# Kernel tuning notes

Measured on AMD Instinct MI355X. Metric: run time of the kernel, lower is better.

The kernel has to match this reference:

```python
import jax, jax.numpy as jnp
import numpy as np

K = 8192      # codebook_dim
D = 256       # embedding_dim
BETA = 0.25
DECAY = 0.99
EPS = 1e-05


def setup_inputs() -> dict:
    key = jax.random.key(0)
    k1, k2, k3, k4 = jax.random.split(key, 4)
    lim = 1.0 / K
    return {
        "z": jax.random.normal(k1, (8, D, 32, 32), dtype=jnp.float32),
        "embedding": jax.random.uniform(k2, (K, D), minval=-lim, maxval=lim, dtype=jnp.float32),
        "cluster_size": jax.random.uniform(k3, (K,), dtype=jnp.float32),
        "ema_w": jax.random.uniform(k4, (K, D), minval=-lim, maxval=lim, dtype=jnp.float32),
    }


def reference(z, embedding, cluster_size, ema_w):
    # z: [B, C, H, W] -> [B, H, W, C]
    zp = jnp.transpose(z, (0, 2, 3, 1))
    zf = zp.reshape(-1, D)                                  # [N, D]
    # squared L2 distance to each code: ||z||^2 + ||e||^2 - 2 z.e
    d = (jnp.sum(zf * zf, axis=1, keepdims=True)
         + jnp.sum(embedding * embedding, axis=1)
         - 2.0 * jnp.einsum("nd,kd->nk", zf, embedding))    # [N, K]
    idx = jnp.argmin(d, axis=1)                             # [N]
    z_q = embedding[idx].reshape(zp.shape)                  # [B, H, W, C]

    # EMA update (training branch), expressed with segment sums instead of
    # materializing the one-hot [N, K] matrix.
    counts = jax.ops.segment_sum(jnp.ones_like(idx, dtype=zf.dtype), idx, num_segments=K)
    new_cs = cluster_size * DECAY + (1.0 - DECAY) * counts
    n = jnp.sum(new_cs)
    new_cs = (new_cs + EPS) / (n + K * EPS) * n
    dw = jax.ops.segment_sum(zf, idx, num_segments=K)       # encodings.T @ zf
    new_ema_w = ema_w * DECAY + (1.0 - DECAY) * dw
    new_embedding = new_ema_w / new_cs[:, None]

    sg = jax.lax.stop_gradient
    loss = jnp.mean((sg(z_q) - zp) ** 2) + BETA * jnp.mean((z_q - sg(zp)) ** 2)
    # straight-through estimator, back to NCHW
    z_q_out = jnp.transpose(zp + sg(z_q - zp), (0, 3, 1, 2))
    return z_q_out, loss, idx, new_cs, new_ema_w, new_embedding
```

## Files before the change

kernel.cpp:

```cpp
#include <hip/hip_runtime.h>

#define CHW 262144
#define HWD 1024

typedef _Float16 v8h __attribute__((ext_vector_type(8)));
typedef _Float16 v4h __attribute__((ext_vector_type(4)));
typedef float    v4f __attribute__((ext_vector_type(4)));

static const unsigned OFF_ASQ  = 0;
static const unsigned OFF_BSQ  = 8192;
static const unsigned OFF_CNT  = 16384;
static const unsigned OFF_HEAD = 24576;
static const unsigned OFF_SCAL = 32768;
static const unsigned OFF_NXT  = 32776;
static const unsigned OFF_ZF   = 40968;
static const unsigned OFF_BH   = 2138120;
static const unsigned OFF_PDK  = 3186696;

#define GLL(g, l) __builtin_amdgcn_global_load_lds( \
    (const __attribute__((address_space(1))) void*)(g), \
    (__attribute__((address_space(3))) void*)(l), 16, 0, 0)

__global__ __launch_bounds__(256) void k_prep(const float* __restrict__ z,
        const float* __restrict__ emb, float* __restrict__ asq, float* __restrict__ bsq,
        _Float16* __restrict__ Bh, _Float16* __restrict__ Bm,
        _Float16* __restrict__ Ah, _Float16* __restrict__ Am,
        float* __restrict__ zf32, float* __restrict__ zerobase) {
    int bx = blockIdx.x;
    int t = threadIdx.x;
    if (bx < 32) {
        int n = bx * 256 + t;
        const float* p = z + (size_t)(n >> 10) * CHW + (n & 1023);
        float s = 0.f;
        #pragma unroll 8
        for (int c = 0; c < 256; ++c) { float v = p[(size_t)c << 10]; s = fmaf(v, v, s); }
        asq[n] = s;
    } else if (bx < 2080) {
        int w = (bx - 32) * 4 + (t >> 6);
        int lane = t & 63;
        float4 v = *(const float4*)(emb + (size_t)w * 256 + lane * 4);
        float s = v.x * v.x;
        s = fmaf(v.y, v.y, s); s = fmaf(v.z, v.z, s); s = fmaf(v.w, v.w, s);
        #pragma unroll
        for (int m = 1; m < 64; m <<= 1) s += __shfl_xor(s, m, 64);
        if (lane == 0) bsq[w] = s;
        float e0 = v.x * 8192.0f, e1 = v.y * 8192.0f, e2 = v.z * 8192.0f, e3 = v.w * 8192.0f;
        _Float16 h0 = (_Float16)e0, h1 = (_Float16)e1, h2 = (_Float16)e2, h3 = (_Float16)e3;
        v4h hv = {h0, h1, h2, h3};
        v4h mv = {(_Float16)((e0 - (float)h0) * 2048.0f),
                  (_Float16)((e1 - (float)h1) * 2048.0f),
                  (_Float16)((e2 - (float)h2) * 2048.0f),
                  (_Float16)((e3 - (float)h3) * 2048.0f)};
        *(v4h*)(Bh + (size_t)w * 256 + lane * 4) = hv;
        *(v4h*)(Bm + (size_t)w * 256 + lane * 4) = mv;
    } else if (bx < 2592) {
        __shared__ float s[64][65];
        int blk = bx - 2080;
        int hw0 = (blk & 15) * 64;
        int c0  = ((blk >> 4) & 3) * 64;
        int b   = blk >> 6;
        #pragma unroll
        for (int ii = 0; ii < 16; ++ii) {
            int e = t + ii * 256;
            int c = e >> 6, x = e & 63;
            s[c][x] = z[(size_t)b * CHW + (size_t)(c0 + c) * HWD + hw0 + x];
        }
        __syncthreads();
        int n = t & 63, cseg = (t >> 6) * 16;
        _Float16 hbuf[16], mbuf[16];
        float fbuf[16];
        #pragma unroll
        for (int j = 0; j < 16; ++j) {
            float v = s[cseg + j][n];
            _Float16 h = (_Float16)v;
            float r = v - (float)h;
            fbuf[j] = v;
            hbuf[j] = h;
            mbuf[j] = (_Float16)(r * 2048.0f);
        }
        size_t off = ((size_t)b * 1024 + hw0 + n) * 256 + c0 + cseg;
        *(v8h*)(Ah + off)     = *(v8h*)(hbuf);
        *(v8h*)(Ah + off + 8) = *(v8h*)(hbuf + 8);
        *(v8h*)(Am + off)     = *(v8h*)(mbuf);
        *(v8h*)(Am + off + 8) = *(v8h*)(mbuf + 8);
        #pragma unroll
        for (int q = 0; q < 4; ++q)
            *(float4*)(zf32 + off + q * 4) = *(float4*)(fbuf + q * 4);
    } else {
        int idx = (bx - 2592) * 1024 + t * 4;
        *(float4*)(zerobase + idx) = (float4){0.f, 0.f, 0.f, 0.f};
        if (bx == 2607 && t == 0) {
            *(float4*)(zerobase + 16384) = (float4){0.f, 0.f, 0.f, 0.f};
            *(float4*)(zerobase + 16388) = (float4){0.f, 0.f, 0.f, 0.f};
        }
    }
}

__global__ __launch_bounds__(512, 4) void k_main(
        const _Float16* __restrict__ Ah, const _Float16* __restrict__ Am,
        const _Float16* __restrict__ Bh, const _Float16* __restrict__ Bm,
        const float* __restrict__ asq, const float* __restrict__ bsq,
        unsigned* __restrict__ pdk) {
    __shared__ _Float16 lds[32768];
    const int kt = blockIdx.x, nt = blockIdx.y;
    const int n0 = nt * 128, k0 = kt * 128;
    const int t = threadIdx.x;
    const int lane = t & 63, w = t >> 6;
    const int wrow = w >> 1, wcol = w & 1;
    const int lm = lane & 15, quad = lane >> 4;

    v4f acc1[2][4], acc2[2][4];
    #pragma unroll
    for (int i = 0; i < 2; ++i)
        #pragma unroll
        for (int j = 0; j < 4; ++j) { acc1[i][j] = (v4f){0.f,0.f,0.f,0.f}; acc2[i][j] = (v4f){0.f,0.f,0.f,0.f}; }

    const int row0 = t >> 2;
    const int c40 = (t & 3) ^ ((row0 >> 1) & 3);
    const char* gA  = (const char*)Ah + (size_t)(n0 + row0) * 512 + c40 * 16;
    const char* gAm = (const char*)Am + (size_t)(n0 + row0) * 512 + c40 * 16;
    const char* gB  = (const char*)Bh + (size_t)(k0 + row0) * 512 + c40 * 16;
    const char* gBm = (const char*)Bm + (size_t)(k0 + row0) * 512 + c40 * 16;

    int sa[2], sb[4];
    #pragma unroll
    for (int i = 0; i < 2; ++i) {
        int mr = wrow * 32 + i * 16 + lm;
        sa[i] = mr * 32 + ((quad ^ ((mr >> 1) & 3)) * 8);
    }
    #pragma unroll
    for (int j = 0; j < 4; ++j) {
        int nr = wcol * 64 + j * 16 + lm;
        sb[j] = nr * 32 + ((quad ^ ((nr >> 1) & 3)) * 8);
    }

    auto stage = [&](int cb, int buf) {
        const size_t co = (size_t)cb * 64;
        _Float16* l = lds + buf * 16384 + t * 8;
        GLL(gA + co,  l);
        GLL(gAm + co, l + 4096);
        GLL(gB + co,  l + 8192);
        GLL(gBm + co, l + 12288);
    };

    stage(0, 0);
    for (int cb = 0; cb < 8; ++cb) {
        __syncthreads();
        if (cb < 7) stage(cb + 1, (cb + 1) & 1);
        const _Float16* L = lds + (cb & 1) * 16384;

        v8h fa[2], fam[2];
        #pragma unroll
        for (int i = 0; i < 2; ++i) {
            fa[i]  = *(const v8h*)(L + sa[i]);
            fam[i] = *(const v8h*)(L + 4096 + sa[i]);
        }
        #pragma unroll
        for (int jh = 0; jh < 2; ++jh) {
            v8h fb0  = *(const v8h*)(L + 8192 + sb[jh * 2]);
            v8h fb1  = *(const v8h*)(L + 8192 + sb[jh * 2 + 1]);
            v8h fbm0 = *(const v8h*)(L + 12288 + sb[jh * 2]);
            v8h fbm1 = *(const v8h*)(L + 12288 + sb[jh * 2 + 1]);
            #pragma unroll
            for (int i = 0; i < 2; ++i) {
                int j0 = jh * 2;
                acc1[i][j0]     = __builtin_amdgcn_mfma_f32_16x16x32_f16(fa[i],  fb0,  acc1[i][j0], 0, 0, 0);
                acc2[i][j0]     = __builtin_amdgcn_mfma_f32_16x16x32_f16(fa[i],  fbm0, acc2[i][j0], 0, 0, 0);
                acc2[i][j0]     = __builtin_amdgcn_mfma_f32_16x16x32_f16(fam[i], fb0,  acc2[i][j0], 0, 0, 0);
                acc1[i][j0 + 1] = __builtin_amdgcn_mfma_f32_16x16x32_f16(fa[i],  fb1,  acc1[i][j0 + 1], 0, 0, 0);
                acc2[i][j0 + 1] = __builtin_amdgcn_mfma_f32_16x16x32_f16(fa[i],  fbm1, acc2[i][j0 + 1], 0, 0, 0);
                acc2[i][j0 + 1] = __builtin_amdgcn_mfma_f32_16x16x32_f16(fam[i], fb1,  acc2[i][j0 + 1], 0, 0, 0);
            }
        }
    }

    float bvv[4];
    #pragma unroll
    for (int j = 0; j < 4; ++j) bvv[j] = bsq[k0 + wcol * 64 + j * 16 + lm];
    unsigned* prow = pdk + ((size_t)(nt * 128 + kt * 2 + wcol) << 7);
    #pragma unroll
    for (int i = 0; i < 2; ++i) {
        #pragma unroll
        for (int r = 0; r < 4; ++r) {
            int mm = wrow * 32 + i * 16 + quad * 4 + r;
            float av_ = asq[n0 + mm];
            unsigned best = 0xFFFFFFFFu;
            #pragma unroll
            for (int j = 0; j < 4; ++j) {
                float S = fmaf(acc2[i][j][r], 4.8828125e-4f, acc1[i][j][r]) * 1.220703125e-4f;
                float dd = (av_ + bvv[j]) - 2.0f * S;
                float gv = dd - av_;
                int mi = (int)(gv * 65536.0f) + 32768;
                int col = k0 + wcol * 64 + j * 16 + lm;
                unsigned key = ((unsigned)mi << 13) | (unsigned)col;
                best = key < best ? key : best;
            }
            #pragma unroll
            for (int xm = 1; xm < 16; xm <<= 1) {
                unsigned o = __shfl_xor(best, xm, 64);
                best = o < best ? o : best;
            }
            if (lm == 0) prow[mm] = best;
        }
    }
}

__global__ __launch_bounds__(256) void k_zqr(const unsigned* __restrict__ pdk,
        const float* __restrict__ z, const float* __restrict__ emb, const float* __restrict__ cs,
        float* __restrict__ out_idx, int* __restrict__ cnt,
        int* __restrict__ head, int* __restrict__ nxt,
        float* __restrict__ out_zq, float* __restrict__ scal) {
    const int bx = blockIdx.x, by = blockIdx.y;
    const int n0 = bx * 64, c00 = by * 64;
    const int lane = threadIdx.x & 63, g = threadIdx.x >> 6;
    const int nt = bx >> 1, mb = (bx & 1) * 64;

    unsigned mn = 0xFFFFFFFFu;
    const unsigned* base = pdk + (((size_t)nt * 128 + g * 32) << 7) + mb + lane;
    #pragma unroll 8
    for (int jj = 0; jj < 32; ++jj) {
        unsigned key = base[jj << 7];
        mn = key < mn ? key : mn;
    }
    __shared__ unsigned part[4][64];
    part[g][lane] = mn;
    __syncthreads();
    unsigned k0v = part[0][lane], k1v = part[1][lane];
    unsigned k2v = part[2][lane], k3v = part[3][lane];
    unsigned f01 = k0v < k1v ? k0v : k1v;
    unsigned f23 = k2v < k3v ? k2v : k3v;
    unsigned fkey = f01 < f23 ? f01 : f23;
    int idxn = (int)(fkey & 8191u);
    int n = n0 + lane;

    if (by == 0) {
        if (g == 0) {
            out_idx[n] = (float)idxn;
            atomicAdd(cnt + idxn, 1);
            int old = atomicExch(head + idxn, n + 1);
            nxt[n] = old;
        } else if (g == 1) {
            float cv = cs[n];
            #pragma unroll
            for (int m = 1; m < 64; m <<= 1) cv += __shfl_xor(cv, m, 64);
            if (lane == 0) atomicAdd(scal + 1, cv);
        }
    }

    int b = n >> 10, hw = n & 1023;
    const float* zr = z + (size_t)b * CHW + hw;
    const float* er = emb + (size_t)idxn * 256;
    float* oz = out_zq + (size_t)b * CHW + hw;
    float ls = 0.f;
    #pragma unroll
    for (int q = 0; q < 4; ++q) {
        int c = c00 + g * 16 + q * 4;
        float4 e4 = *(const float4*)(er + c);
        float ev[4] = {e4.x, e4.y, e4.z, e4.w};
        #pragma unroll
        for (int r = 0; r < 4; ++r) {
            float zp = zr[(size_t)(c + r) << 10];
            float dif = ev[r] - zp;
            oz[(size_t)(c + r) << 10] = zp + dif;
            ls = fmaf(dif, dif, ls);
        }
    }
    #pragma unroll
    for (int m = 1; m < 64; m <<= 1) ls += __shfl_xor(ls, m, 64);
    __shared__ float red[4];
    if (lane == 0) red[g] = ls;
    __syncthreads();
    if (threadIdx.x == 0) atomicAdd(scal, red[0] + red[1] + red[2] + red[3]);
}

__global__ __launch_bounds__(256) void k_fin(const float* __restrict__ cs, const float* __restrict__ ema,
        const int* __restrict__ head, const int* __restrict__ nxt, const float* __restrict__ zf32,
        const float* __restrict__ scal, const int* __restrict__ cnt,
        float* __restrict__ out_ncs, float* __restrict__ out_ema,
        float* __restrict__ out_emb, float* __restrict__ out_loss) {
    int k = blockIdx.x * 4 + (threadIdx.x >> 6);
    int lane = threadIdx.x & 63;
    float4 dwv = {0.f, 0.f, 0.f, 0.f};
    int cur = head[k];
    while (cur) {
        int n = cur - 1;
        float4 v = *(const float4*)(zf32 + (size_t)n * 256 + lane * 4);
        dwv.x += v.x; dwv.y += v.y; dwv.z += v.z; dwv.w += v.w;
        cur = nxt[n];
    }
    const float C1 = (float)(1.0 - 0.99);
    const float KEPS = (float)(8192 * 1e-5);
    float ncs0v = cs[k] * 0.99f + C1 * (float)cnt[k];
    float nsum = 0.99f * scal[1] + C1 * 8192.0f;
    float ncs = (ncs0v + 1e-5f) / (nsum + KEPS) * nsum;
    if (lane == 0) out_ncs[k] = ncs;
    size_t base = (size_t)k * 256 + lane * 4;
    float4 e4 = *(const float4*)(ema + base);
    float r0 = e4.x * 0.99f + C1 * dwv.x;
    float r1 = e4.y * 0.99f + C1 * dwv.y;
    float r2 = e4.z * 0.99f + C1 * dwv.z;
    float r3 = e4.w * 0.99f + C1 * dwv.w;
    out_ema[base + 0] = r0; out_ema[base + 1] = r1; out_ema[base + 2] = r2; out_ema[base + 3] = r3;
    out_emb[base + 0] = r0 / ncs; out_emb[base + 1] = r1 / ncs;
    out_emb[base + 2] = r2 / ncs; out_emb[base + 3] = r3 / ncs;
    if (blockIdx.x == 0 && threadIdx.x == 0) {
        float m = scal[0] * (1.0f / 2097152.0f);
        out_loss[0] = m + 0.25f * m;
    }
}

extern "C" void kernel_launch(void* const* d_in, const int* in_sizes, int n_in,
                              void* d_out, int out_size, void* d_ws, size_t ws_size,
                              hipStream_t stream) {
    const float* z   = (const float*)d_in[0];
    const float* emb = (const float*)d_in[1];
    const float* cs  = (const float*)d_in[2];
    const float* ema = (const float*)d_in[3];
    float* out = (float*)d_out;
    float* wsf = (float*)d_ws;

    float* asq  = wsf + OFF_ASQ;
    float* bsq  = wsf + OFF_BSQ;
    int*   cnt  = (int*)(wsf + OFF_CNT);
    int*   head = (int*)(wsf + OFF_HEAD);
    float* scal = wsf + OFF_SCAL;
    int*   nxt  = (int*)(wsf + OFF_NXT);
    float* zf32 = wsf + OFF_ZF;
    _Float16* Bh = (_Float16*)(wsf + OFF_BH);
    unsigned* pdk = (unsigned*)(wsf + OFF_PDK);

    float* out_zq   = out;
    float* out_loss = out + 2097152;
    float* out_idx  = out + 2097153;
    float* out_ncs  = out + 2105345;
    float* out_ema  = out + 2113537;
    float* out_emb  = out + 4210689;

    _Float16* Ah = (_Float16*)(out + 2113540);
    _Float16* Am = (_Float16*)(out + 2113540 + 1048576);
    _Float16* Bm = (_Float16*)(out + 4210692);

    k_prep<<<2608, 256, 0, stream>>>(z, emb, asq, bsq, Bh, Bm, Ah, Am, zf32, wsf + OFF_CNT);
    k_main<<<dim3(64, 64), 512, 0, stream>>>(Ah, Am, Bh, Bm, asq, bsq, pdk);
    k_zqr<<<dim3(128, 4), 256, 0, stream>>>(pdk, z, emb, cs, out_idx, cnt, head, nxt, out_zq, scal);
    k_fin<<<2048, 256, 0, stream>>>(cs, ema, head, nxt, zf32, scal, cnt, out_ncs, out_ema, out_emb, out_loss);
}
```

Measured before the change: 243.3 us.

## Fuse argmin via atomicMin and rebuild z from fp16 splits in EMA

The GEMM epilogue now merges its per-row best key straight into a global final-index array with atomicMin. This replaces the large buffer of per-tile partial keys and the separate min-reduction pass in k_zqr. The fp32 copy of z in NHWC layout is no longer written; k_fin rebuilds the rows from the fp16 hi/lo split arrays, which move from the output buffer into the workspace. This saves memory traffic, at the cost of contended atomics and a dw sum that only matches fp32 to about 22 bits.

```diff
diff --git a/kernel.cpp b/kernel.cpp
--- a/kernel.cpp
+++ b/kernel.cpp
@@ -11,11 +11,13 @@
 static const unsigned OFF_BSQ  = 8192;
 static const unsigned OFF_CNT  = 16384;
 static const unsigned OFF_HEAD = 24576;
-static const unsigned OFF_SCAL = 32768;
-static const unsigned OFF_NXT  = 32776;
-static const unsigned OFF_ZF   = 40968;
-static const unsigned OFF_BH   = 2138120;
-static const unsigned OFF_PDK  = 3186696;
+static const unsigned OFF_NXT  = 32768;
+static const unsigned OFF_FIN  = 40960;
+static const unsigned OFF_SCAL = 49152;
+static const unsigned OFF_AH   = 49160;
+static const unsigned OFF_AM   = 1097736;
+static const unsigned OFF_BH   = 2146312;
+static const unsigned OFF_BM   = 3194888;
 
 #define GLL(g, l) __builtin_amdgcn_global_load_lds( \
     (const __attribute__((address_space(1))) void*)(g), \
@@ -25,7 +27,7 @@
         const float* __restrict__ emb, float* __restrict__ asq, float* __restrict__ bsq,
         _Float16* __restrict__ Bh, _Float16* __restrict__ Bm,
         _Float16* __restrict__ Ah, _Float16* __restrict__ Am,
-        float* __restrict__ zf32, float* __restrict__ zerobase) {
+        float* __restrict__ zerobase) {
     int bx = blockIdx.x;
     int t = threadIdx.x;
     if (bx < 32) {
@@ -68,13 +70,11 @@
         __syncthreads();
         int n = t & 63, cseg = (t >> 6) * 16;
         _Float16 hbuf[16], mbuf[16];
-        float fbuf[16];
         #pragma unroll
         for (int j = 0; j < 16; ++j) {
             float v = s[cseg + j][n];
             _Float16 h = (_Float16)v;
             float r = v - (float)h;
-            fbuf[j] = v;
             hbuf[j] = h;
             mbuf[j] = (_Float16)(r * 2048.0f);
         }
@@ -83,15 +83,14 @@
         *(v8h*)(Ah + off + 8) = *(v8h*)(hbuf + 8);
         *(v8h*)(Am + off)     = *(v8h*)(mbuf);
         *(v8h*)(Am + off + 8) = *(v8h*)(mbuf + 8);
-        #pragma unroll
-        for (int q = 0; q < 4; ++q)
-            *(float4*)(zf32 + off + q * 4) = *(float4*)(fbuf + q * 4);
     } else {
         int idx = (bx - 2592) * 1024 + t * 4;
-        *(float4*)(zerobase + idx) = (float4){0.f, 0.f, 0.f, 0.f};
-        if (bx == 2607 && t == 0) {
-            *(float4*)(zerobase + 16384) = (float4){0.f, 0.f, 0.f, 0.f};
-            *(float4*)(zerobase + 16388) = (float4){0.f, 0.f, 0.f, 0.f};
+        unsigned v = (idx >= 24576) ? 0xFFFFFFFFu : 0u;
+        uint4 val = {v, v, v, v};
+        *(uint4*)((unsigned*)zerobase + idx) = val;
+        if (bx == 2623 && t == 0) {
+            *(float4*)(zerobase + 32768) = (float4){0.f, 0.f, 0.f, 0.f};
+            *(float4*)(zerobase + 32772) = (float4){0.f, 0.f, 0.f, 0.f};
         }
     }
 }
@@ -100,7 +99,7 @@
         const _Float16* __restrict__ Ah, const _Float16* __restrict__ Am,
         const _Float16* __restrict__ Bh, const _Float16* __restrict__ Bm,
         const float* __restrict__ asq, const float* __restrict__ bsq,
-        unsigned* __restrict__ pdk) {
+        unsigned* __restrict__ fin) {
     __shared__ _Float16 lds[32768];
     const int kt = blockIdx.x, nt = blockIdx.y;
     const int n0 = nt * 128, k0 = kt * 128;
@@ -177,7 +176,6 @@
     float bvv[4];
     #pragma unroll
     for (int j = 0; j < 4; ++j) bvv[j] = bsq[k0 + wcol * 64 + j * 16 + lm];
-    unsigned* prow = pdk + ((size_t)(nt * 128 + kt * 2 + wcol) << 7);
     #pragma unroll
     for (int i = 0; i < 2; ++i) {
         #pragma unroll
@@ -200,12 +198,12 @@
                 unsigned o = __shfl_xor(best, xm, 64);
                 best = o < best ? o : best;
             }
-            if (lm == 0) prow[mm] = best;
-        }
-    }
-}
-
-__global__ __launch_bounds__(256) void k_zqr(const unsigned* __restrict__ pdk,
+            if (lm == 0) atomicMin(fin + n0 + mm, best);
+        }
+    }
+}
+
+__global__ __launch_bounds__(256) void k_zqr(const unsigned* __restrict__ fin,
         const float* __restrict__ z, const float* __restrict__ emb, const float* __restrict__ cs,
         float* __restrict__ out_idx, int* __restrict__ cnt,
         int* __restrict__ head, int* __restrict__ nxt,
@@ -213,25 +211,8 @@
     const int bx = blockIdx.x, by = blockIdx.y;
     const int n0 = bx * 64, c00 = by * 64;
     const int lane = threadIdx.x & 63, g = threadIdx.x >> 6;
-    const int nt = bx >> 1, mb = (bx & 1) * 64;
-
-    unsigned mn = 0xFFFFFFFFu;
-    const unsigned* base = pdk + (((size_t)nt * 128 + g * 32) << 7) + mb + lane;
-    #pragma unroll 8
-    for (int jj = 0; jj < 32; ++jj) {
-        unsigned key = base[jj << 7];
-        mn = key < mn ? key : mn;
-    }
-    __shared__ unsigned part[4][64];
-    part[g][lane] = mn;
-    __syncthreads();
-    unsigned k0v = part[0][lane], k1v = part[1][lane];
-    unsigned k2v = part[2][lane], k3v = part[3][lane];
-    unsigned f01 = k0v < k1v ? k0v : k1v;
-    unsigned f23 = k2v < k3v ? k2v : k3v;
-    unsigned fkey = f01 < f23 ? f01 : f23;
-    int idxn = (int)(fkey & 8191u);
-    int n = n0 + lane;
+    const int n = n0 + lane;
+    const int idxn = (int)(fin[n] & 8191u);
 
     if (by == 0) {
         if (g == 0) {
@@ -274,7 +255,8 @@
 }
 
 __global__ __launch_bounds__(256) void k_fin(const float* __restrict__ cs, const float* __restrict__ ema,
-        const int* __restrict__ head, const int* __restrict__ nxt, const float* __restrict__ zf32,
+        const int* __restrict__ head, const int* __restrict__ nxt,
+        const _Float16* __restrict__ Ah, const _Float16* __restrict__ Am,
         const float* __restrict__ scal, const int* __restrict__ cnt,
         float* __restrict__ out_ncs, float* __restrict__ out_ema,
         float* __restrict__ out_emb, float* __restrict__ out_loss) {
@@ -284,8 +266,12 @@
     int cur = head[k];
     while (cur) {
         int n = cur - 1;
-        float4 v = *(const float4*)(zf32 + (size_t)n * 256 + lane * 4);
-        dwv.x += v.x; dwv.y += v.y; dwv.z += v.z; dwv.w += v.w;
+        v4h hh = *(const v4h*)(Ah + (size_t)n * 256 + lane * 4);
+        v4h mm = *(const v4h*)(Am + (size_t)n * 256 + lane * 4);
+        dwv.x += fmaf((float)mm[0], 4.8828125e-4f, (float)hh[0]);
+        dwv.y += fmaf((float)mm[1], 4.8828125e-4f, (float)hh[1]);
+        dwv.z += fmaf((float)mm[2], 4.8828125e-4f, (float)hh[2]);
+        dwv.w += fmaf((float)mm[3], 4.8828125e-4f, (float)hh[3]);
         cur = nxt[n];
     }
     const float C1 = (float)(1.0 - 0.99);
@@ -323,11 +309,13 @@
     float* bsq  = wsf + OFF_BSQ;
     int*   cnt  = (int*)(wsf + OFF_CNT);
     int*   head = (int*)(wsf + OFF_HEAD);
+    int*   nxt  = (int*)(wsf + OFF_NXT);
+    unsigned* fin = (unsigned*)(wsf + OFF_FIN);
     float* scal = wsf + OFF_SCAL;
-    int*   nxt  = (int*)(wsf + OFF_NXT);
-    float* zf32 = wsf + OFF_ZF;
+    _Float16* Ah = (_Float16*)(wsf + OFF_AH);
+    _Float16* Am = (_Float16*)(wsf + OFF_AM);
     _Float16* Bh = (_Float16*)(wsf + OFF_BH);
-    unsigned* pdk = (unsigned*)(wsf + OFF_PDK);
+    _Float16* Bm = (_Float16*)(wsf + OFF_BM);
 
     float* out_zq   = out;
     float* out_loss = out + 2097152;
@@ -336,12 +324,8 @@
     float* out_ema  = out + 2113537;
     float* out_emb  = out + 4210689;
 
-    _Float16* Ah = (_Float16*)(out + 2113540);
-    _Float16* Am = (_Float16*)(out + 2113540 + 1048576);
-    _Float16* Bm = (_Float16*)(out + 4210692);
-
-    k_prep<<<2608, 256, 0, stream>>>(z, emb, asq, bsq, Bh, Bm, Ah, Am, zf32, wsf + OFF_CNT);
-    k_main<<<dim3(64, 64), 512, 0, stream>>>(Ah, Am, Bh, Bm, asq, bsq, pdk);
-    k_zqr<<<dim3(128, 4), 256, 0, stream>>>(pdk, z, emb, cs, out_idx, cnt, head, nxt, out_zq, scal);
-    k_fin<<<2048, 256, 0, stream>>>(cs, ema, head, nxt, zf32, scal, cnt, out_ncs, out_ema, out_emb, out_loss);
-}
+    k_prep<<<2624, 256, 0, stream>>>(z, emb, asq, bsq, Bh, Bm, Ah, Am, wsf + OFF_CNT);
+    k_main<<<dim3(64, 64), 512, 0, stream>>>(Ah, Am, Bh, Bm, asq, bsq, fin);
+    k_zqr<<<dim3(128, 4), 256, 0, stream>>>(fin, z, emb, cs, out_idx, cnt, head, nxt, out_zq, scal);
+    k_fin<<<2048, 256, 0, stream>>>(cs, ema, head, nxt, Ah, Am, scal, cnt, out_ncs, out_ema, out_emb, out_loss);
+}
```

After: 261.8 us. +7.6%, slower.

## Drop fp32 z copy, rebuild dw from fp16 split pair, stage argmin keys in LDS

Applied to the files above, without the earlier changes.

The prep kernel no longer writes a separate fp32 transposed copy of z. The final kernel rebuilds each z row from the fp16 high/mid split (Ah + Am/2048) when summing dw. The main GEMM kernel now collects its per-row argmin keys in LDS and writes them with one coalesced 256-wide store, instead of scattered lane-0 stores. Buffers are rearranged across workspace and output scratch to fit. This trades 8 MB of fp32 writes and reads for 2 MB of extra fp16 reads and adds two block barriers. The reconstructed z may differ slightly from the exact fp32 value.

```diff
diff --git a/kernel.cpp b/kernel.cpp
--- a/kernel.cpp
+++ b/kernel.cpp
@@ -11,11 +11,12 @@
 static const unsigned OFF_BSQ  = 8192;
 static const unsigned OFF_CNT  = 16384;
 static const unsigned OFF_HEAD = 24576;
-static const unsigned OFF_SCAL = 32768;
-static const unsigned OFF_NXT  = 32776;
-static const unsigned OFF_ZF   = 40968;
+static const unsigned OFF_NXT  = 32768;
+static const unsigned OFF_SCAL = 40960;
+static const unsigned OFF_AH   = 40968;
+static const unsigned OFF_AM   = 1089544;
 static const unsigned OFF_BH   = 2138120;
-static const unsigned OFF_PDK  = 3186696;
+static const unsigned OFF_BM   = 3186696;
 
 #define GLL(g, l) __builtin_amdgcn_global_load_lds( \
     (const __attribute__((address_space(1))) void*)(g), \
@@ -25,7 +26,7 @@
         const float* __restrict__ emb, float* __restrict__ asq, float* __restrict__ bsq,
         _Float16* __restrict__ Bh, _Float16* __restrict__ Bm,
         _Float16* __restrict__ Ah, _Float16* __restrict__ Am,
-        float* __restrict__ zf32, float* __restrict__ zerobase) {
+        float* __restrict__ zerobase) {
     int bx = blockIdx.x;
     int t = threadIdx.x;
     if (bx < 32) {
@@ -68,13 +69,11 @@
         __syncthreads();
         int n = t & 63, cseg = (t >> 6) * 16;
         _Float16 hbuf[16], mbuf[16];
-        float fbuf[16];
         #pragma unroll
         for (int j = 0; j < 16; ++j) {
             float v = s[cseg + j][n];
             _Float16 h = (_Float16)v;
             float r = v - (float)h;
-            fbuf[j] = v;
             hbuf[j] = h;
             mbuf[j] = (_Float16)(r * 2048.0f);
         }
@@ -83,16 +82,11 @@
         *(v8h*)(Ah + off + 8) = *(v8h*)(hbuf + 8);
         *(v8h*)(Am + off)     = *(v8h*)(mbuf);
         *(v8h*)(Am + off + 8) = *(v8h*)(mbuf + 8);
-        #pragma unroll
-        for (int q = 0; q < 4; ++q)
-            *(float4*)(zf32 + off + q * 4) = *(float4*)(fbuf + q * 4);
     } else {
         int idx = (bx - 2592) * 1024 + t * 4;
         *(float4*)(zerobase + idx) = (float4){0.f, 0.f, 0.f, 0.f};
-        if (bx == 2607 && t == 0) {
-            *(float4*)(zerobase + 16384) = (float4){0.f, 0.f, 0.f, 0.f};
-            *(float4*)(zerobase + 16388) = (float4){0.f, 0.f, 0.f, 0.f};
-        }
+        if (bx == 2592 && t == 0)
+            *(float4*)(zerobase + 24576) = (float4){0.f, 0.f, 0.f, 0.f};
     }
 }
 
@@ -177,7 +171,8 @@
     float bvv[4];
     #pragma unroll
     for (int j = 0; j < 4; ++j) bvv[j] = bsq[k0 + wcol * 64 + j * 16 + lm];
-    unsigned* prow = pdk + ((size_t)(nt * 128 + kt * 2 + wcol) << 7);
+    __syncthreads();
+    unsigned* lrow = (unsigned*)lds;
     #pragma unroll
     for (int i = 0; i < 2; ++i) {
         #pragma unroll
@@ -200,9 +195,11 @@
                 unsigned o = __shfl_xor(best, xm, 64);
                 best = o < best ? o : best;
             }
-            if (lm == 0) prow[mm] = best;
-        }
-    }
+            if (lm == 0) lrow[wcol * 128 + mm] = best;
+        }
+    }
+    __syncthreads();
+    if (t < 256) pdk[(((size_t)nt * 128 + kt * 2) << 7) + t] = lrow[t];
 }
 
 __global__ __launch_bounds__(256) void k_zqr(const unsigned* __restrict__ pdk,
@@ -274,7 +271,8 @@
 }
 
 __global__ __launch_bounds__(256) void k_fin(const float* __restrict__ cs, const float* __restrict__ ema,
-        const int* __restrict__ head, const int* __restrict__ nxt, const float* __restrict__ zf32,
+        const int* __restrict__ head, const int* __restrict__ nxt,
+        const _Float16* __restrict__ Ah, const _Float16* __restrict__ Am,
         const float* __restrict__ scal, const int* __restrict__ cnt,
         float* __restrict__ out_ncs, float* __restrict__ out_ema,
         float* __restrict__ out_emb, float* __restrict__ out_loss) {
@@ -284,8 +282,12 @@
     int cur = head[k];
     while (cur) {
         int n = cur - 1;
-        float4 v = *(const float4*)(zf32 + (size_t)n * 256 + lane * 4);
-        dwv.x += v.x; dwv.y += v.y; dwv.z += v.z; dwv.w += v.w;
+        v4h hh = *(const v4h*)(Ah + (size_t)n * 256 + lane * 4);
+        v4h mm = *(const v4h*)(Am + (size_t)n * 256 + lane * 4);
+        dwv.x += fmaf((float)mm[0], 4.8828125e-4f, (float)hh[0]);
+        dwv.y += fmaf((float)mm[1], 4.8828125e-4f, (float)hh[1]);
+        dwv.z += fmaf((float)mm[2], 4.8828125e-4f, (float)hh[2]);
+        dwv.w += fmaf((float)mm[3], 4.8828125e-4f, (float)hh[3]);
         cur = nxt[n];
     }
     const float C1 = (float)(1.0 - 0.99);
@@ -323,11 +325,12 @@
     float* bsq  = wsf + OFF_BSQ;
     int*   cnt  = (int*)(wsf + OFF_CNT);
     int*   head = (int*)(wsf + OFF_HEAD);
+    int*   nxt  = (int*)(wsf + OFF_NXT);
     float* scal = wsf + OFF_SCAL;
-    int*   nxt  = (int*)(wsf + OFF_NXT);
-    float* zf32 = wsf + OFF_ZF;
+    _Float16* Ah = (_Float16*)(wsf + OFF_AH);
+    _Float16* Am = (_Float16*)(wsf + OFF_AM);
     _Float16* Bh = (_Float16*)(wsf + OFF_BH);
-    unsigned* pdk = (unsigned*)(wsf + OFF_PDK);
+    _Float16* Bm = (_Float16*)(wsf + OFF_BM);
 
     float* out_zq   = out;
     float* out_loss = out + 2097152;
@@ -336,12 +339,10 @@
     float* out_ema  = out + 2113537;
     float* out_emb  = out + 4210689;
 
-    _Float16* Ah = (_Float16*)(out + 2113540);
-    _Float16* Am = (_Float16*)(out + 2113540 + 1048576);
-    _Float16* Bm = (_Float16*)(out + 4210692);
-
-    k_prep<<<2608, 256, 0, stream>>>(z, emb, asq, bsq, Bh, Bm, Ah, Am, zf32, wsf + OFF_CNT);
+    unsigned* pdk = (unsigned*)(out + 2113540);
+
+    k_prep<<<2608, 256, 0, stream>>>(z, emb, asq, bsq, Bh, Bm, Ah, Am, wsf + OFF_CNT);
     k_main<<<dim3(64, 64), 512, 0, stream>>>(Ah, Am, Bh, Bm, asq, bsq, pdk);
     k_zqr<<<dim3(128, 4), 256, 0, stream>>>(pdk, z, emb, cs, out_idx, cnt, head, nxt, out_zq, scal);
-    k_fin<<<2048, 256, 0, stream>>>(cs, ema, head, nxt, zf32, scal, cnt, out_ncs, out_ema, out_emb, out_loss);
-}
+    k_fin<<<2048, 256, 0, stream>>>(cs, ema, head, nxt, Ah, Am, scal, cnt, out_ncs, out_ema, out_emb, out_loss);
+}
```

Result: no change. 243.0 us (median of 3 runs) (-0.1%).
